# Kernel tuning notes

Measured on AMD Instinct MI355X. Metric: run time of the kernel, lower is better.

The kernel has to match this reference:

```python
import jax, jax.numpy as jnp
import numpy as np

NUM_HEADS = 16
EPS = 1e-05


def setup_inputs() -> dict:
    key = jax.random.key(0)
    k1, k2, k3 = jax.random.split(key, 3)
    b, n, d = 2, 2048, 1024
    x = jax.random.normal(k1, (b, n, d), dtype=jnp.float32)
    # nn.Linear weights stored here as (in, out); scaled like typical init
    wqkv = jax.random.normal(k2, (d, 3 * d), dtype=jnp.float32) * (1.0 / np.sqrt(d))
    wo = jax.random.normal(k3, (d, d), dtype=jnp.float32) * (1.0 / np.sqrt(d))
    return {"x": x, "wqkv": wqkv, "wo": wo}


def reference(x, wqkv, wo):
    b, n, d = x.shape
    h = NUM_HEADS
    hd = d // h
    qkv = x @ wqkv                      # (b, n, 3d)
    q, k, v = jnp.split(qkv, 3, axis=-1)
    q = jax.nn.relu(q)
    k = jax.nn.relu(k)
    # (b, n, h*hd) -> (b, h, n, hd)
    split_heads = lambda t: t.reshape(b, n, h, hd).transpose(0, 2, 1, 3)
    q, k, v = split_heads(q), split_heads(k), split_heads(v)
    # cumulative outer products: kv[b,h,t] = sum_{s<=t} k_s (x) v_s  -> (b,h,n,hd,hd)
    kv = jnp.cumsum(k[..., :, None] * v[..., None, :], axis=2)
    num = jnp.einsum('bhnd,bhnde->bhne', q, kv)          # (b, h, n, hd)
    k_sum = jnp.cumsum(k, axis=2)                        # (b, h, n, hd)
    den = jnp.einsum('bhnd,bhnd->bhn', q, k_sum)[..., None] + EPS
    y = num / den                                        # (b, h, n, hd)
    y = y.transpose(0, 2, 1, 3).reshape(b, n, d)         # merge heads
    return y @ wo
```

## Files before the change

kernel.cpp:

```cpp
#include <hip/hip_runtime.h>
#include <hip/hip_bf16.h>

#define SEQ    2048
#define DMODEL 1024
#define NHEADS 16
#define HD     64
#define CS     64
#define NC     (SEQ / CS)
#define STSZ   (HD * HD + HD)
#define EPS_LA 1e-5f
#define LP     72

typedef __attribute__((ext_vector_type(8))) short  bf16x8;
typedef __attribute__((ext_vector_type(8))) unsigned short ushort8;
typedef __attribute__((ext_vector_type(4))) float  f32x4;

__device__ __forceinline__ void gload_lds16(const void* g, void* l) {
  __builtin_amdgcn_global_load_lds(
      (const __attribute__((address_space(1))) void*)g,
      (__attribute__((address_space(3))) void*)l, 16, 0, 0);
}

__device__ __forceinline__ ushort f2bf(float x) {
  __hip_bfloat16 h = __float2bfloat16(x);
  return __builtin_bit_cast(ushort, h);
}
__device__ __forceinline__ float bf2f(ushort u) {
  unsigned int v = ((unsigned int)u) << 16;
  return __builtin_bit_cast(float, v);
}

__global__ __launch_bounds__(256) void conv_bf16(
    const float* __restrict__ src, ushort* __restrict__ dst) {
  const int i = blockIdx.x * 256 + threadIdx.x;
  float4 v = *(const float4*)(src + (size_t)i * 4);
  ushort4 o;
  o.x = f2bf(v.x); o.y = f2bf(v.y); o.z = f2bf(v.z); o.w = f2bf(v.w);
  *(ushort4*)(dst + (size_t)i * 4) = o;
}

__global__ __launch_bounds__(256) void transpose_to_bf16(
    const float* __restrict__ src, ushort* __restrict__ dst, int R, int Ncols) {
  __shared__ float t[64][65];
  const int r0 = blockIdx.y * 64, c0 = blockIdx.x * 64;
  const int tid = threadIdx.x;
  const int lr = tid >> 2;
  const int lc = (tid & 3) * 16;
  const float* sp = src + (size_t)(r0 + lr) * Ncols + c0 + lc;
  #pragma unroll
  for (int j = 0; j < 4; ++j) {
    float4 v = *(const float4*)(sp + j * 4);
    t[lr][lc + j * 4 + 0] = v.x;
    t[lr][lc + j * 4 + 1] = v.y;
    t[lr][lc + j * 4 + 2] = v.z;
    t[lr][lc + j * 4 + 3] = v.w;
  }
  __syncthreads();
  ushort out[16];
  #pragma unroll
  for (int j = 0; j < 16; ++j)
    out[j] = f2bf(t[lc + j][lr]);
  ushort* dp = dst + (size_t)(c0 + lr) * R + r0 + lc;
  *(uint4*)dp = *(const uint4*)&out[0];
  *(uint4*)(dp + 8) = *(const uint4*)&out[8];
}

template <bool OUT_BF16>
__global__ __launch_bounds__(256) void gemm_swz(
    const ushort* __restrict__ A, const ushort* __restrict__ Bt,
    void* __restrict__ Cv, int M, int N, int K, int relu_limit) {
  __shared__ ushort Asm[128 * 64];
  __shared__ ushort Bsm[128 * 64];

  const int tid  = threadIdx.x;
  const int lane = tid & 63;
  const int w    = tid >> 6;
  const int wr   = w >> 1, wc = w & 1;
  const int brow = blockIdx.y * 128;
  const int bcol = blockIdx.x * 128;

  f32x4 acc[4][4];
  #pragma unroll
  for (int i = 0; i < 4; ++i)
    #pragma unroll
    for (int j = 0; j < 4; ++j) acc[i][j] = (f32x4)0.f;

  const int r8   = lane >> 3;
  const int arow = w * 32 + r8;
  const int acol = ((lane & 7) ^ r8) * 8;
  const ushort* Ag = A  + (size_t)(brow + arow) * K + acol;
  const ushort* Bg = Bt + (size_t)(bcol + arow) * K + acol;

  const int l15 = lane & 15;
  const int khi = (lane >> 4) * 8;

  for (int k0 = 0; k0 < K; k0 += 64) {
    #pragma unroll
    for (int u = 0; u < 4; ++u) {
      gload_lds16(Ag + k0 + (size_t)u * 8 * K, &Asm[(w * 4 + u) * 512]);
      gload_lds16(Bg + k0 + (size_t)u * 8 * K, &Bsm[(w * 4 + u) * 512]);
    }
    __syncthreads();
    #pragma unroll
    for (int kk = 0; kk < 2; ++kk) {
      const int ko = kk * 32 + khi;
      bf16x8 af[4], bfr[4];
      #pragma unroll
      for (int mi = 0; mi < 4; ++mi) {
        const int row = wr * 64 + mi * 16 + l15;
        af[mi] = *(const bf16x8*)&Asm[row * 64 + (ko ^ ((row & 7) << 3))];
      }
      #pragma unroll
      for (int ni = 0; ni < 4; ++ni) {
        const int row = wc * 64 + ni * 16 + l15;
        bfr[ni] = *(const bf16x8*)&Bsm[row * 64 + (ko ^ ((row & 7) << 3))];
      }
      #pragma unroll
      for (int mi = 0; mi < 4; ++mi)
        #pragma unroll
        for (int ni = 0; ni < 4; ++ni)
          acc[mi][ni] = __builtin_amdgcn_mfma_f32_16x16x32_bf16(
              af[mi], bfr[ni], acc[mi][ni], 0, 0, 0);
    }
    __syncthreads();
  }

  #pragma unroll
  for (int mi = 0; mi < 4; ++mi) {
    #pragma unroll
    for (int ni = 0; ni < 4; ++ni) {
      const int r0  = brow + wr * 64 + mi * 16 + (lane >> 4) * 4;
      const int col = bcol + wc * 64 + ni * 16 + l15;
      const bool rl = col < relu_limit;
      #pragma unroll
      for (int i = 0; i < 4; ++i) {
        float v = acc[mi][ni][i];
        if (rl) v = fmaxf(v, 0.f);
        if (OUT_BF16)
          ((ushort*)Cv)[(size_t)(r0 + i) * N + col] = f2bf(v);
        else
          ((float*)Cv)[(size_t)(r0 + i) * N + col] = v;
      }
    }
  }
}

__global__ __launch_bounds__(256) void chunk_sums_mfma(
    const ushort* __restrict__ qkvb, float* __restrict__ state) {
  __shared__ ushort Kt[64 * LP];
  __shared__ ushort Vt[64 * LP];

  const int bh = blockIdx.x >> 5;
  const int c  = blockIdx.x & (NC - 1);
  const int b  = bh >> 4;
  const int h  = bh & (NHEADS - 1);
  const int tid = threadIdx.x;

  const size_t rs   = 3 * DMODEL;
  const size_t base = ((size_t)(b * SEQ + c * CS)) * rs + (size_t)h * HD;

  const int r  = tid >> 2;
  const int sg = (tid & 3) * 16;
  {
    const ushort* src = qkvb + base + (size_t)r * rs + sg;
    ushort8 k0 = *(const ushort8*)(src + DMODEL);
    ushort8 k1 = *(const ushort8*)(src + DMODEL + 8);
    ushort8 v0 = *(const ushort8*)(src + 2 * DMODEL);
    ushort8 v1 = *(const ushort8*)(src + 2 * DMODEL + 8);
    #pragma unroll
    for (int j = 0; j < 8; ++j) {
      Kt[(sg + j) * LP + r]     = k0[j];
      Kt[(sg + 8 + j) * LP + r] = k1[j];
      Vt[(sg + j) * LP + r]     = v0[j];
      Vt[(sg + 8 + j) * LP + r] = v1[j];
    }
  }
  __syncthreads();

  const int lane = tid & 63;
  const int w    = tid >> 6;
  const int l15  = lane & 15;
  const int khi  = (lane >> 4) * 8;

  bf16x8 va[2];
  #pragma unroll
  for (int kk = 0; kk < 2; ++kk)
    va[kk] = *(const bf16x8*)&Vt[(w * 16 + l15) * LP + kk * 32 + khi];

  f32x4 a[4];
  #pragma unroll
  for (int ct = 0; ct < 4; ++ct) {
    a[ct] = (f32x4)0.f;
    #pragma unroll
    for (int kk = 0; kk < 2; ++kk)
      a[ct] = __builtin_amdgcn_mfma_f32_16x16x32_bf16(
          va[kk], *(const bf16x8*)&Kt[(ct * 16 + l15) * LP + kk * 32 + khi],
          a[ct], 0, 0, 0);
  }

  float* st = state + (size_t)blockIdx.x * STSZ;
  #pragma unroll
  for (int ct = 0; ct < 4; ++ct) {
    #pragma unroll
    for (int i = 0; i < 4; ++i) {
      const int e = w * 16 + (lane >> 4) * 4 + i;
      const int d = ct * 16 + l15;
      st[e * HD + d] = a[ct][i];
    }
  }

  if (tid < HD) {
    float s = 0.f;
    #pragma unroll 8
    for (int t = 0; t < CS; ++t) s += bf2f(Kt[tid * LP + t]);
    st[HD * HD + tid] = s;
  }
}

__global__ __launch_bounds__(256) void chunk_prefix(float* __restrict__ state) {
  const int g = blockIdx.x * 256 + threadIdx.x;
  const int total = 2 * NHEADS * STSZ;
  if (g >= total) return;
  const int bh   = g / STSZ;
  const int elem = g - bh * STSZ;
  float* p = state + (size_t)bh * NC * STSZ + elem;

  float vals[NC];
  #pragma unroll
  for (int c = 0; c < NC; ++c) vals[c] = p[(size_t)c * STSZ];
  float run = 0.f;
  #pragma unroll
  for (int c = 0; c < NC; ++c) {
    const float t = vals[c];
    p[(size_t)c * STSZ] = run;
    run += t;
  }
}

__global__ __launch_bounds__(256) void chunk_out_mfma(
    const ushort* __restrict__ qkvb, const float* __restrict__ state,
    ushort* __restrict__ y) {
  __shared__ ushort Qs[64 * LP];
  __shared__ ushort Ks[64 * LP];
  __shared__ ushort Vt[80 * LP];
  __shared__ ushort Kv[80 * LP];
  __shared__ ushort Sm[64 * LP];

  const int bh = blockIdx.x >> 5;
  const int c  = blockIdx.x & (NC - 1);
  const int b  = bh >> 4;
  const int h  = bh & (NHEADS - 1);
  const int tid = threadIdx.x;

  const size_t rs   = 3 * DMODEL;
  const size_t base = ((size_t)(b * SEQ + c * CS)) * rs + (size_t)h * HD;

  {
    const int r  = tid >> 2;
    const int sg = (tid & 3) * 16;
    const ushort* src = qkvb + base + (size_t)r * rs + sg;
    ushort8 q0 = *(const ushort8*)(src);
    ushort8 q1 = *(const ushort8*)(src + 8);
    ushort8 k0 = *(const ushort8*)(src + DMODEL);
    ushort8 k1 = *(const ushort8*)(src + DMODEL + 8);
    ushort8 v0 = *(const ushort8*)(src + 2 * DMODEL);
    ushort8 v1 = *(const ushort8*)(src + 2 * DMODEL + 8);
    *(ushort8*)&Qs[r * LP + sg]     = q0;
    *(ushort8*)&Qs[r * LP + sg + 8] = q1;
    *(ushort8*)&Ks[r * LP + sg]     = k0;
    *(ushort8*)&Ks[r * LP + sg + 8] = k1;
    #pragma unroll
    for (int j = 0; j < 8; ++j) {
      Vt[(sg + j) * LP + r]     = v0[j];
      Vt[(sg + 8 + j) * LP + r] = v1[j];
    }
  }
  {
    const int idx = tid * 4;
    const int row = 64 + (idx >> 6);
    const int col = idx & 63;
    const ushort val = (row == 64) ? (ushort)0x3F80 : (ushort)0;
    ushort4 v4 = {val, val, val, val};
    *(ushort4*)&Vt[row * LP + col] = v4;
  }
  {
    const float* sp = state + ((size_t)bh * NC + c) * STSZ;
    const int off = tid * 16;
    const int e   = off >> 6;
    const int col = off & 63;
    ushort tmp[16];
    #pragma unroll
    for (int j = 0; j < 4; ++j) {
      float4 f = *(const float4*)(sp + off + j * 4);
      tmp[j * 4 + 0] = f2bf(f.x);
      tmp[j * 4 + 1] = f2bf(f.y);
      tmp[j * 4 + 2] = f2bf(f.z);
      tmp[j * 4 + 3] = f2bf(f.w);
    }
    *(ushort8*)&Kv[e * LP + col]     = *(const ushort8*)&tmp[0];
    *(ushort8*)&Kv[e * LP + col + 8] = *(const ushort8*)&tmp[8];
    if (tid < 16) {
      const int c4 = tid * 4;
      ushort4 v4;
      v4.x = f2bf(sp[HD * HD + c4 + 0]);
      v4.y = f2bf(sp[HD * HD + c4 + 1]);
      v4.z = f2bf(sp[HD * HD + c4 + 2]);
      v4.w = f2bf(sp[HD * HD + c4 + 3]);
      *(ushort4*)&Kv[64 * LP + c4] = v4;
    }
    if (tid < 240) {
      const int idx = tid * 4;
      const int row = 65 + (idx >> 6);
      const int col2 = idx & 63;
      ushort4 z = {0, 0, 0, 0};
      *(ushort4*)&Kv[row * LP + col2] = z;
    }
  }
  __syncthreads();

  const int lane = tid & 63;
  const int w    = tid >> 6;
  const int l15  = lane & 15;
  const int khi  = (lane >> 4) * 8;

  bf16x8 qa[2];
  #pragma unroll
  for (int kk = 0; kk < 2; ++kk)
    qa[kk] = *(const bf16x8*)&Qs[(w * 16 + l15) * LP + kk * 32 + khi];

  {
    f32x4 sac[4];
    #pragma unroll
    for (int ct = 0; ct < 4; ++ct) {
      sac[ct] = (f32x4)0.f;
      #pragma unroll
      for (int kk = 0; kk < 2; ++kk)
        sac[ct] = __builtin_amdgcn_mfma_f32_16x16x32_bf16(
            qa[kk], *(const bf16x8*)&Ks[(ct * 16 + l15) * LP + kk * 32 + khi],
            sac[ct], 0, 0, 0);
    }
    const int t0 = w * 16 + (lane >> 4) * 4;
    #pragma unroll
    for (int ct = 0; ct < 4; ++ct) {
      const int s = ct * 16 + l15;
      #pragma unroll
      for (int i = 0; i < 4; ++i) {
        const int t = t0 + i;
        const float v = (s <= t) ? sac[ct][i] : 0.f;
        Sm[t * LP + s] = f2bf(v);
      }
    }
  }
  __syncthreads();

  bf16x8 sa[2];
  #pragma unroll
  for (int kk = 0; kk < 2; ++kk)
    sa[kk] = *(const bf16x8*)&Sm[(w * 16 + l15) * LP + kk * 32 + khi];

  f32x4 o[5];
  #pragma unroll
  for (int ct = 0; ct < 5; ++ct) {
    o[ct] = (f32x4)0.f;
    #pragma unroll
    for (int kk = 0; kk < 2; ++kk)
      o[ct] = __builtin_amdgcn_mfma_f32_16x16x32_bf16(
          qa[kk], *(const bf16x8*)&Kv[(ct * 16 + l15) * LP + kk * 32 + khi],
          o[ct], 0, 0, 0);
    #pragma unroll
    for (int kk = 0; kk < 2; ++kk)
      o[ct] = __builtin_amdgcn_mfma_f32_16x16x32_bf16(
          sa[kk], *(const bf16x8*)&Vt[(ct * 16 + l15) * LP + kk * 32 + khi],
          o[ct], 0, 0, 0);
  }

  float den[4];
  #pragma unroll
  for (int i = 0; i < 4; ++i)
    den[i] = __shfl(o[4][i], lane & 48) + EPS_LA;

  const int t0 = w * 16 + (lane >> 4) * 4;
  #pragma unroll
  for (int ct = 0; ct < 4; ++ct) {
    const int e = ct * 16 + l15;
    #pragma unroll
    for (int i = 0; i < 4; ++i) {
      const int t = t0 + i;
      y[((size_t)(b * SEQ + c * CS + t)) * DMODEL + (size_t)h * HD + e] =
          f2bf(o[ct][i] / den[i]);
    }
  }
}

extern "C" void kernel_launch(void* const* d_in, const int* in_sizes, int n_in,
                              void* d_out, int out_size, void* d_ws,
                              size_t ws_size, hipStream_t stream) {
  (void)in_sizes; (void)n_in; (void)out_size; (void)ws_size;
  const float* x    = (const float*)d_in[0];
  const float* wqkv = (const float*)d_in[1];
  const float* wo   = (const float*)d_in[2];
  float* out = (float*)d_out;

  const int M  = 2 * SEQ;
  const int K  = DMODEL;
  const int N1 = 3 * DMODEL;
  const int N2 = DMODEL;

  float*  state = (float*)d_ws;
  ushort* qkvb  = (ushort*)(state + (size_t)2 * NHEADS * NC * STSZ);
  ushort* xb    = qkvb + (size_t)M * N1;
  ushort* yb    = xb + (size_t)M * K;
  ushort* wqkvT = yb + (size_t)M * K;
  ushort* woT   = wqkvT + (size_t)K * N1;

  dim3 blk(256);

  conv_bf16<<<dim3((M * K) / 1024), blk, 0, stream>>>(x, xb);
  transpose_to_bf16<<<dim3(N1 / 64, K / 64), blk, 0, stream>>>(wqkv, wqkvT, K, N1);
  transpose_to_bf16<<<dim3(N2 / 64, K / 64), blk, 0, stream>>>(wo, woT, K, N2);

  gemm_swz<true><<<dim3(N1 / 128, M / 128), blk, 0, stream>>>(
      xb, wqkvT, qkvb, M, N1, K, 2 * DMODEL);

  chunk_sums_mfma<<<dim3(2 * NHEADS * NC), blk, 0, stream>>>(qkvb, state);

  const int total = 2 * NHEADS * STSZ;
  chunk_prefix<<<dim3((total + 255) / 256), blk, 0, stream>>>(state);

  chunk_out_mfma<<<dim3(2 * NHEADS * NC), blk, 0, stream>>>(qkvb, state, yb);

  gemm_swz<false><<<dim3(N2 / 128, M / 128), blk, 0, stream>>>(
      yb, woT, out, M, N2, K, 0);
}
```

Before: 97.38 us.

## Add 256x256 double-buffered 8-wave GEMM with XCD remap for QKV projection

Replaces the 128x128 single-buffered QKV GEMM with a new 512-thread kernel using 256x256 output tiles, double-buffered LDS filled by direct global-to-LDS loads interleaved across four phases, and a block-index remap that spreads consecutive tiles across the eight XCDs. Larger tiles raise operand reuse per LDS load, and prefetching the next K tile during MFMA work hides memory latency. It also raises MFMA priority with s_setprio. The cost is 128KB of LDS per block and higher register pressure, and the grid shrinks to 192 blocks, which may underfill the 256 CUs.

```diff
diff --git a/kernel.cpp b/kernel.cpp
--- a/kernel.cpp
+++ b/kernel.cpp
@@ -63,6 +63,113 @@
   ushort* dp = dst + (size_t)(c0 + lr) * R + r0 + lc;
   *(uint4*)dp = *(const uint4*)&out[0];
   *(uint4*)(dp + 8) = *(const uint4*)&out[8];
+}
+
+template <bool OUT_BF16>
+__global__ __launch_bounds__(512, 2) void gemm_8ph(
+    const ushort* __restrict__ A, const ushort* __restrict__ Bt,
+    void* __restrict__ Cv, int M, int N, int K, int relu_limit, int nbx) {
+  __shared__ ushort Asm[2][256 * 64];
+  __shared__ ushort Bsm[2][256 * 64];
+
+  int wg = blockIdx.x;
+  const int cpx = gridDim.x >> 3;
+  wg = (wg & 7) * cpx + (wg >> 3);
+  const int bx = wg % nbx;
+  const int by = wg / nbx;
+  const int brow = by * 256;
+  const int bcol = bx * 256;
+
+  const int tid  = threadIdx.x;
+  const int lane = tid & 63;
+  const int w    = tid >> 6;
+  const int wm   = w >> 2;
+  const int wn   = w & 3;
+  const int l15  = lane & 15;
+  const int khi  = (lane >> 4) * 8;
+  const int r8   = lane >> 3;
+  const int acol = ((lane & 7) ^ r8) * 8;
+
+  const ushort* Ag = A  + (size_t)(brow + w * 8 + r8) * K + acol;
+  const ushort* Bg = Bt + (size_t)(bcol + w * 8 + r8) * K + acol;
+
+  f32x4 acc[8][4];
+  #pragma unroll
+  for (int i = 0; i < 8; ++i)
+    #pragma unroll
+    for (int j = 0; j < 4; ++j) acc[i][j] = (f32x4)0.f;
+
+  #pragma unroll
+  for (int u = 0; u < 4; ++u) {
+    gload_lds16(Ag + (size_t)u * 64 * K, &Asm[0][(u * 8 + w) * 512]);
+    gload_lds16(Bg + (size_t)u * 64 * K, &Bsm[0][(u * 8 + w) * 512]);
+  }
+  __syncthreads();
+
+  const int NT = K >> 6;
+  int cur = 0;
+  for (int kt = 0; kt < NT; ++kt) {
+    const ushort* An = Ag + (size_t)(kt + 1) * 64;
+    const ushort* Bn = Bg + (size_t)(kt + 1) * 64;
+    const bool pf = (kt + 1 < NT);
+    #pragma unroll
+    for (int ph = 0; ph < 4; ++ph) {
+      const int rh = ph >> 1, ch = ph & 1;
+      bf16x8 af[4][2], bfr[2][2];
+      #pragma unroll
+      for (int i = 0; i < 4; ++i) {
+        const int r = wm * 128 + (rh * 4 + i) * 16 + l15;
+        #pragma unroll
+        for (int ks = 0; ks < 2; ++ks)
+          af[i][ks] = *(const bf16x8*)
+              &Asm[cur][r * 64 + ((ks * 32 + khi) ^ ((r & 7) << 3))];
+      }
+      #pragma unroll
+      for (int j = 0; j < 2; ++j) {
+        const int rn = wn * 64 + (ch * 2 + j) * 16 + l15;
+        #pragma unroll
+        for (int ks = 0; ks < 2; ++ks)
+          bfr[j][ks] = *(const bf16x8*)
+              &Bsm[cur][rn * 64 + ((ks * 32 + khi) ^ ((rn & 7) << 3))];
+      }
+      if (pf) {
+        gload_lds16(An + (size_t)ph * 64 * K, &Asm[cur ^ 1][(ph * 8 + w) * 512]);
+        gload_lds16(Bn + (size_t)ph * 64 * K, &Bsm[cur ^ 1][(ph * 8 + w) * 512]);
+      }
+      __builtin_amdgcn_s_barrier();
+      __builtin_amdgcn_s_setprio(1);
+      #pragma unroll
+      for (int i = 0; i < 4; ++i)
+        #pragma unroll
+        for (int j = 0; j < 2; ++j)
+          #pragma unroll
+          for (int ks = 0; ks < 2; ++ks)
+            acc[rh * 4 + i][ch * 2 + j] = __builtin_amdgcn_mfma_f32_16x16x32_bf16(
+                af[i][ks], bfr[j][ks], acc[rh * 4 + i][ch * 2 + j], 0, 0, 0);
+      __builtin_amdgcn_s_setprio(0);
+    }
+    __syncthreads();
+    cur ^= 1;
+  }
+
+  #pragma unroll
+  for (int fr = 0; fr < 8; ++fr) {
+    #pragma unroll
+    for (int fc = 0; fc < 4; ++fc) {
+      const int r0  = brow + wm * 128 + fr * 16 + (lane >> 4) * 4;
+      const int col = bcol + wn * 64 + fc * 16 + l15;
+      const bool rl = col < relu_limit;
+      #pragma unroll
+      for (int i = 0; i < 4; ++i) {
+        float v = acc[fr][fc][i];
+        if (rl) v = fmaxf(v, 0.f);
+        if (OUT_BF16)
+          ((ushort*)Cv)[(size_t)(r0 + i) * N + col] = f2bf(v);
+        else
+          ((float*)Cv)[(size_t)(r0 + i) * N + col] = v;
+      }
+    }
+  }
 }
 
 template <bool OUT_BF16>
@@ -419,8 +526,8 @@
   transpose_to_bf16<<<dim3(N1 / 64, K / 64), blk, 0, stream>>>(wqkv, wqkvT, K, N1);
   transpose_to_bf16<<<dim3(N2 / 64, K / 64), blk, 0, stream>>>(wo, woT, K, N2);
 
-  gemm_swz<true><<<dim3(N1 / 128, M / 128), blk, 0, stream>>>(
-      xb, wqkvT, qkvb, M, N1, K, 2 * DMODEL);
+  gemm_8ph<true><<<dim3((M / 256) * (N1 / 256)), dim3(512), 0, stream>>>(
+      xb, wqkvT, qkvb, M, N1, K, 2 * DMODEL, N1 / 256);
 
   chunk_sums_mfma<<<dim3(2 * NHEADS * NC), blk, 0, stream>>>(qkvb, state);
 
```

Measured after the change: 99.95 us. +2.6%, slower.
